# Kernel optimization log

Hardware: AMD Instinct MI355X
Metric: run time of the kernel (lower is better)

## Reference

```python
import jax, jax.numpy as jnp
import numpy as np

B, H, W, C = 1, 72, 72, 768
NH, HD = 12, 64
FF = 3072
EPS = 1e-6
THETA = 10000.0
S = H * W


def _rope_tables():
    freqs = 1.0 / THETA ** (np.arange(0, HD, 4, dtype=np.float32) / HD)  # [16]
    t = np.arange(H, dtype=np.float32)
    fx = np.outer(t, freqs)  # [72,16]
    fy = np.outer(t, freqs)
    fx = np.tile(fx[:, None, :], (1, W, 1))  # [72,72,16]
    fy = np.tile(fy[None, :, :], (H, 1, 1))
    fxy = np.concatenate([fx, fy], axis=-1).reshape(S, -1)  # [5184,32]
    fxy = np.repeat(fxy, 2, axis=-1)  # [5184,64]
    return jnp.asarray(np.cos(fxy)), jnp.asarray(np.sin(fxy))


def _rotate_pairwise(x):
    x1 = x[..., ::2]
    x2 = x[..., 1::2]
    return jnp.stack([-x2, x1], axis=-1).reshape(x.shape)


def _layernorm(x, g, b):
    m = jnp.mean(x, axis=-1, keepdims=True)
    v = jnp.mean(jnp.square(x - m), axis=-1, keepdims=True)
    return (x - m) * jax.lax.rsqrt(v + EPS) * g + b


def setup_inputs() -> dict:
    key = jax.random.key(0)
    ks = jax.random.split(key, 12)
    s_c = 1.0 / np.sqrt(C)
    s_ff = 1.0 / np.sqrt(FF)
    d = {
        "hidden_states": jax.random.normal(ks[0], (B, H, W, C), jnp.float32),
        "wq": jax.random.normal(ks[1], (C, C), jnp.float32) * s_c,
        "bq": jnp.zeros((C,), jnp.float32),
        "wk": jax.random.normal(ks[2], (C, C), jnp.float32) * s_c,
        "bk": jnp.zeros((C,), jnp.float32),
        "wv": jax.random.normal(ks[3], (C, C), jnp.float32) * s_c,
        "bv": jnp.zeros((C,), jnp.float32),
        "wo": jax.random.normal(ks[4], (C, C), jnp.float32) * s_c,
        "bo": jnp.zeros((C,), jnp.float32),
        "g1": jnp.ones((C,), jnp.float32),
        "b1": jnp.zeros((C,), jnp.float32),
        "g2": jnp.ones((C,), jnp.float32),
        "b2": jnp.zeros((C,), jnp.float32),
        "w_fc1": jax.random.normal(ks[5], (C, FF), jnp.float32) * s_c,
        "b_fc1": jnp.zeros((FF,), jnp.float32),
        "w_fc2": jax.random.normal(ks[6], (FF, C), jnp.float32) * s_ff,
        "b_fc2": jnp.zeros((C,), jnp.float32),
        "ls1": jnp.full((C,), 1e-5, jnp.float32),
        "ls2": jnp.full((C,), 1e-5, jnp.float32),
    }
    return d


def reference(hidden_states, wq, bq, wk, bk, wv, bv, wo, bo, g1, b1, g2, b2,
              w_fc1, b_fc1, w_fc2, b_fc2, ls1, ls2):
    cos, sin = _rope_tables()  # [S, HD]
    cos = cos[None, None]  # [1,1,S,HD]
    sin = sin[None, None]

    residual = hidden_states
    x = hidden_states.reshape(B, S, C)
    x = _layernorm(x, g1, b1)

    # attention
    q = (x @ wq + bq).reshape(B, S, NH, HD).transpose(0, 2, 1, 3)
    k = (x @ wk + bk).reshape(B, S, NH, HD).transpose(0, 2, 1, 3)
    v = (x @ wv + bv).reshape(B, S, NH, HD).transpose(0, 2, 1, 3)
    q = q * cos + _rotate_pairwise(q) * sin
    k = k * cos + _rotate_pairwise(k) * sin
    scale = HD ** -0.5
    attn = jax.nn.softmax(jnp.einsum('bhqd,bhkd->bhqk', q, k) * scale, axis=-1)
    o = jnp.einsum('bhqk,bhkd->bhqd', attn, v)
    o = o.transpose(0, 2, 1, 3).reshape(B, S, C)
    o = o @ wo + bo
    o = o * ls1

    hs = residual + o.reshape(B, H, W, C)
    residual = hs
    x = _layernorm(hs.reshape(B, S, C), g2, b2)
    x = jax.nn.gelu(x @ w_fc1 + b_fc1, approximate=False)
    x = x @ w_fc2 + b_fc2
    x = x * ls2
    return residual + x.reshape(B, H, W, C)
```

## Files before the change

kernel.cpp:

```cpp
#include <hip/hip_runtime.h>

#define S_  5184
#define C_  768
#define NH_ 12
#define HD_ 64
#define FF_ 3072
#define WW_ 72

typedef __attribute__((ext_vector_type(8))) short bf16x8;
typedef __attribute__((ext_vector_type(4))) float f32x4;

__device__ __forceinline__ float bf2f(unsigned short u){
    unsigned int i = ((unsigned int)u) << 16; float f; __builtin_memcpy(&f,&i,4); return f;
}
__device__ __forceinline__ unsigned short f2bf(float f){
    unsigned int i; __builtin_memcpy(&i,&f,4);
    unsigned int r = (i + 0x7fffu + ((i>>16)&1u)) >> 16;
    return (unsigned short)r;
}
__device__ __forceinline__ float ldf(float v){ return v; }
__device__ __forceinline__ float ldf(unsigned short v){ return bf2f(v); }

__device__ __forceinline__ void gload16(const void* g, const void* l) {
    __builtin_amdgcn_global_load_lds((const __attribute__((address_space(1))) void*)g,
                                     (__attribute__((address_space(3))) void*)l, 16, 0, 0);
}
__device__ __forceinline__ unsigned int cvtpk(float lo, float hi){
    unsigned int r;
    asm volatile("v_cvt_pk_bf16_f32 %0, %1, %2" : "=v"(r) : "v"(lo), "v"(hi));
    return r;
}

template<typename TIN>
__global__ __launch_bounds__(256) void ln_k(const TIN* __restrict__ x,
                                            const float* __restrict__ g,
                                            const float* __restrict__ b,
                                            unsigned short* __restrict__ out)
{
    int row = blockIdx.x, tid = threadIdx.x;
    const TIN* xr = x + (size_t)row * C_;
    float v0 = ldf(xr[tid]), v1 = ldf(xr[tid+256]), v2 = ldf(xr[tid+512]);
    float s = v0+v1+v2, q = v0*v0+v1*v1+v2*v2;
    #pragma unroll
    for (int off=32; off; off>>=1){ s += __shfl_xor(s,off); q += __shfl_xor(q,off); }
    __shared__ float ss[4], qq[4], mshare[2];
    int lane = tid & 63, wv = tid >> 6;
    if (!lane){ ss[wv] = s; qq[wv] = q; }
    __syncthreads();
    if (!tid){
        float S2 = ss[0]+ss[1]+ss[2]+ss[3];
        float Q2 = qq[0]+qq[1]+qq[2]+qq[3];
        float mean = S2 * (1.f/C_);
        float var  = Q2 * (1.f/C_) - mean*mean;
        mshare[0] = mean; mshare[1] = rsqrtf(var + 1e-6f);
    }
    __syncthreads();
    float mean = mshare[0], inv = mshare[1];
    unsigned short* orow = out + (size_t)row * C_;
    orow[tid]     = f2bf((v0-mean)*inv*g[tid]     + b[tid]);
    orow[tid+256] = f2bf((v1-mean)*inv*g[tid+256] + b[tid+256]);
    orow[tid+512] = f2bf((v2-mean)*inv*g[tid+512] + b[tid+512]);
}

__global__ __launch_bounds__(256) void rope_tables_k(float* __restrict__ cosT,
                                                     float* __restrict__ sinT)
{
    int idx = blockIdx.x * 256 + threadIdx.x;
    if (idx >= S_*32) return;
    int s = idx >> 5, i = idx & 31;
    int hh = s / WW_, ww = s % WW_;
    int m = i & 15;
    float coord = (i < 16) ? (float)hh : (float)ww;
    float freq = powf(10000.0f, -(float)m / 16.0f);
    float a = coord * freq;
    float c = cosf(a), sn = sinf(a);
    cosT[s*64 + 2*i]   = c;  cosT[s*64 + 2*i+1] = c;
    sinT[s*64 + 2*i]   = sn; sinT[s*64 + 2*i+1] = sn;
}

__global__ __launch_bounds__(256) void rope_apply_k(unsigned short* __restrict__ q,
                                                    unsigned short* __restrict__ k,
                                                    const float* __restrict__ cosT,
                                                    const float* __restrict__ sinT)
{
    int idx = blockIdx.x * 256 + threadIdx.x;
    if (idx >= S_*NH_*32) return;
    int s = idx / (NH_*32);
    int p = idx % (NH_*32);
    int h = p >> 5, i = p & 31;
    size_t base = (size_t)s*C_ + h*HD_ + 2*i;
    float c = cosT[s*64 + 2*i], sn = sinT[s*64 + 2*i];
    float x0 = bf2f(q[base]), x1 = bf2f(q[base+1]);
    q[base]   = f2bf((x0*c - x1*sn) * 0.125f);
    q[base+1] = f2bf((x1*c + x0*sn) * 0.125f);
    x0 = bf2f(k[base]); x1 = bf2f(k[base+1]);
    k[base]   = f2bf(x0*c - x1*sn);
    k[base+1] = f2bf(x1*c + x0*sn);
}

__global__ __launch_bounds__(256) void transpose_w(const float* __restrict__ W,
                                                   unsigned short* __restrict__ WT,
                                                   int K, int N)
{
    __shared__ float t[32][33];
    int tx = threadIdx.x, ty = threadIdx.y;
    int n0 = blockIdx.x * 32, k0 = blockIdx.y * 32;
    #pragma unroll
    for (int i = 0; i < 4; i++)
        t[ty + i*8][tx] = W[(size_t)(k0 + ty + i*8)*N + n0 + tx];
    __syncthreads();
    #pragma unroll
    for (int i = 0; i < 4; i++)
        WT[(size_t)(n0 + ty + i*8)*K + k0 + tx] = f2bf(t[tx][ty + i*8]);
}

template<int EPI, int NWC>
__global__ __launch_bounds__(256) void gemm_mfma(const unsigned short* __restrict__ A,
                                                 const unsigned short* __restrict__ BT,
                                                 const float* __restrict__ bias,
                                                 const float* __restrict__ biasB,
                                                 const float* __restrict__ biasC,
                                                 const float* __restrict__ scale,
                                                 const float* __restrict__ addend,
                                                 void* __restrict__ outp,
                                                 void* __restrict__ outp2,
                                                 int M, int N, int K)
{
    const int BN = 64*NWC;
    const int MI = (NWC == 2) ? 4 : 2;
    __shared__ __align__(16) unsigned short As[2][8192];
    __shared__ __align__(16) unsigned short Bs[2][4096*NWC];
    int tid = threadIdx.x;
    int w = tid >> 6, lane = tid & 63, lq = lane & 15, lk = lane >> 4;
    int wr = (NWC == 2) ? (w >> 1) : w;
    int wc = (NWC == 2) ? (w & 1) : 0;
    int bm = blockIdx.y * 128, bn = blockIdx.x * BN;

    f32x4 acc[MI][4];
    #pragma unroll
    for (int i = 0; i < MI; i++)
        #pragma unroll
        for (int j = 0; j < 4; j++) acc[i][j] = 0;

    auto STAGE = [&](int buf, int kt) {
        #pragma unroll
        for (int u = 0; u < 4; u++) {
            int t = w*4 + u;
            int c = t*64 + lane;
            int kg = c >> 7, row = c & 127;
            int ra = bm + row; if (ra >= M) ra = M - 1;
            gload16(A + (size_t)ra*K + kt*64 + kg*8, As[buf] + t*512);
        }
        #pragma unroll
        for (int u = 0; u < 2*NWC; u++) {
            int t = w*2*NWC + u;
            int c = t*64 + lane;
            int kg = (NWC == 2) ? (c >> 7) : (c >> 6);
            int row = (NWC == 2) ? (c & 127) : (c & 63);
            gload16(BT + (size_t)(bn + row)*K + kt*64 + kg*8, Bs[buf] + t*512);
        }
    };

    int nk = K / 64;
    STAGE(0, 0);
    int cur = 0;
    for (int kt = 0; kt < nk; kt++) {
        __syncthreads();
        if (kt + 1 < nk) STAGE(cur ^ 1, kt + 1);
        #pragma unroll
        for (int kk = 0; kk < 2; kk++) {
            bf16x8 af[MI], bfr[4];
            #pragma unroll
            for (int mi = 0; mi < MI; mi++)
                af[mi] = *(const bf16x8*)(As[cur] + (kk*4 + lk)*1024 + (wr*MI*16 + mi*16 + lq)*8);
            #pragma unroll
            for (int ni = 0; ni < 4; ni++)
                bfr[ni] = *(const bf16x8*)(Bs[cur] + (kk*4 + lk)*BN*8 + (wc*64 + ni*16 + lq)*8);
            #pragma unroll
            for (int mi = 0; mi < MI; mi++)
                #pragma unroll
                for (int ni = 0; ni < 4; ni++)
                    acc[mi][ni] = __builtin_amdgcn_mfma_f32_16x16x32_bf16(af[mi], bfr[ni], acc[mi][ni], 0, 0, 0);
        }
        cur ^= 1;
    }

    #pragma unroll
    for (int mi = 0; mi < MI; mi++) {
        #pragma unroll
        for (int ni = 0; ni < 4; ni++) {
            int n = bn + wc*64 + ni*16 + lq;
            int m0 = bm + wr*MI*16 + mi*16 + lk*4;
            if (EPI == 4) {
                if (n < 1536) {
                    const float* bb = (n < 768) ? bias : biasB;
                    int nn = (n < 768) ? n : (n - 768);
                    size_t base = (n < 768) ? 0 : ((size_t)S_ * 768);
                    #pragma unroll
                    for (int r = 0; r < 4; r++) {
                        int m = m0 + r;
                        if (m < M)
                            ((unsigned short*)outp)[base + (size_t)m*768 + nn] = f2bf(acc[mi][ni][r] + bb[nn]);
                    }
                } else {
                    if (m0 < M) {
                        float bv = biasC[n - 1536];
                        ushort4 pv;
                        pv.x = f2bf(acc[mi][ni][0] + bv);
                        pv.y = f2bf(acc[mi][ni][1] + bv);
                        pv.z = f2bf(acc[mi][ni][2] + bv);
                        pv.w = f2bf(acc[mi][ni][3] + bv);
                        *(ushort4*)((unsigned short*)outp2 + (size_t)(n - 1536)*S_ + m0) = pv;
                    }
                }
            } else {
                #pragma unroll
                for (int r = 0; r < 4; r++) {
                    int m = m0 + r;
                    if (m < M) {
                        float v = acc[mi][ni][r] + bias[n];
                        if (EPI == 1) {
                            v = 0.5f * v * (1.f + erff(v * 0.70710678f));
                            ((unsigned short*)outp)[(size_t)m*N + n] = f2bf(v);
                        } else {
                            size_t o = (size_t)m*N + n;
                            ((float*)outp)[o] = v*scale[n] + addend[o];
                        }
                    }
                }
            }
        }
    }
}

__global__ __launch_bounds__(256) void attn_mfma2(const unsigned short* __restrict__ Q,
                                                  const unsigned short* __restrict__ Kb,
                                                  const unsigned short* __restrict__ Vt,
                                                  unsigned short* __restrict__ O)
{
    __shared__ __align__(16) unsigned short Ks[2][4096];
    __shared__ __align__(16) unsigned short Vs[2][4096];
    int tid = threadIdx.x;
    int w = tid >> 6, lane = tid & 63, lq = lane & 15, lk = lane >> 4;
    int h = blockIdx.y;
    int q0 = blockIdx.x * 128 + w * 32;

    bf16x8 qf[2][2];
    #pragma unroll
    for (int qi = 0; qi < 2; qi++) {
        int qr = q0 + qi*16 + lq; if (qr >= S_) qr = S_ - 1;
        #pragma unroll
        for (int ks = 0; ks < 2; ks++)
            qf[qi][ks] = *(const bf16x8*)(Q + (size_t)qr*C_ + h*64 + ks*32 + lk*8);
    }

    f32x4 oacc[2][4];
    #pragma unroll
    for (int qi = 0; qi < 2; qi++)
        #pragma unroll
        for (int df = 0; df < 4; df++) oacc[qi][df] = 0;
    float m_[2] = {-INFINITY, -INFINITY};
    float l_[2] = {0.f, 0.f};

    auto STAGE = [&](int buf, int t) {
        int kv0 = t * 64;
        #pragma unroll
        for (int u = 0; u < 4; u++) {
            int tt = w*4 + u;
            if (tt < 8)
                gload16(Kb + (size_t)(kv0 + lane)*C_ + h*64 + tt*8, Ks[buf] + tt*512);
            else
                gload16(Vt + (size_t)(h*64 + lane)*S_ + kv0 + (tt-8)*8, Vs[buf] + (tt-8)*512);
        }
    };

    const int NT = S_/64;
    STAGE(0, 0);
    int cur = 0;
    for (int t = 0; t < NT; t++) {
        __syncthreads();
        if (t + 1 < NT) STAGE(cur ^ 1, t + 1);

        f32x4 s[2][4];
        #pragma unroll
        for (int qi = 0; qi < 2; qi++)
            #pragma unroll
            for (int nf = 0; nf < 4; nf++) s[qi][nf] = 0;
        #pragma unroll
        for (int ks = 0; ks < 2; ks++) {
            #pragma unroll
            for (int nf = 0; nf < 4; nf++) {
                bf16x8 kf = *(const bf16x8*)(Ks[cur] + (ks*4 + lk)*512 + (nf*16 + lq)*8);
                #pragma unroll
                for (int qi = 0; qi < 2; qi++)
                    s[qi][nf] = __builtin_amdgcn_mfma_f32_16x16x32_bf16(kf, qf[qi][ks], s[qi][nf], 0, 0, 0);
            }
        }

        unsigned int pk[2][8];
        #pragma unroll
        for (int qi = 0; qi < 2; qi++) {
            float tm = -INFINITY;
            #pragma unroll
            for (int nf = 0; nf < 4; nf++)
                #pragma unroll
                for (int r = 0; r < 4; r++) tm = fmaxf(tm, s[qi][nf][r]);
            tm = fmaxf(tm, __shfl_xor(tm, 16));
            tm = fmaxf(tm, __shfl_xor(tm, 32));
            float mn = fmaxf(m_[qi], tm);
            float corr = __expf(m_[qi] - mn);
            m_[qi] = mn;
            float ps = 0.f;
            #pragma unroll
            for (int nf = 0; nf < 4; nf++)
                #pragma unroll
                for (int r = 0; r < 4; r++) {
                    float p = __expf(s[qi][nf][r] - mn);
                    s[qi][nf][r] = p; ps += p;
                }
            ps += __shfl_xor(ps, 16);
            ps += __shfl_xor(ps, 32);
            l_[qi] = l_[qi]*corr + ps;
            #pragma unroll
            for (int df = 0; df < 4; df++)
                #pragma unroll
                for (int r = 0; r < 4; r++) oacc[qi][df][r] *= corr;
            #pragma unroll
            for (int nf = 0; nf < 4; nf++) {
                pk[qi][nf*2+0] = cvtpk(s[qi][nf][0], s[qi][nf][1]);
                pk[qi][nf*2+1] = cvtpk(s[qi][nf][2], s[qi][nf][3]);
            }
        }

        #pragma unroll
        for (int ks = 0; ks < 2; ks++) {
            #pragma unroll
            for (int df = 0; df < 4; df++) {
                int d = df*16 + lq;
                union { bf16x8 v; unsigned long long dd[2]; } va;
                va.dd[0] = *(const unsigned long long*)(Vs[cur] + (4*ks + (lk>>1))*512 + d*8 + (lk&1)*4);
                va.dd[1] = *(const unsigned long long*)(Vs[cur] + (4*ks + 2 + (lk>>1))*512 + d*8 + (lk&1)*4);
                #pragma unroll
                for (int qi = 0; qi < 2; qi++) {
                    union { bf16x8 v; unsigned int u[4]; } pb;
                    pb.u[0] = pk[qi][4*ks+0]; pb.u[1] = pk[qi][4*ks+1];
                    pb.u[2] = pk[qi][4*ks+2]; pb.u[3] = pk[qi][4*ks+3];
                    oacc[qi][df] = __builtin_amdgcn_mfma_f32_16x16x32_bf16(va.v, pb.v, oacc[qi][df], 0, 0, 0);
                }
            }
        }
        cur ^= 1;
    }

    #pragma unroll
    for (int qi = 0; qi < 2; qi++) {
        int q = q0 + qi*16 + lq;
        if (q < S_) {
            float rl = 1.f / l_[qi];
            #pragma unroll
            for (int df = 0; df < 4; df++) {
                ushort4 pv;
                pv.x = f2bf(oacc[qi][df][0] * rl);
                pv.y = f2bf(oacc[qi][df][1] * rl);
                pv.z = f2bf(oacc[qi][df][2] * rl);
                pv.w = f2bf(oacc[qi][df][3] * rl);
                *(ushort4*)(O + (size_t)q*C_ + h*64 + df*16 + lk*4) = pv;
            }
        }
    }
}

extern "C" void kernel_launch(void* const* d_in, const int* in_sizes, int n_in,
                              void* d_out, int out_size, void* d_ws, size_t ws_size,
                              hipStream_t stream)
{
    const float* hidden = (const float*)d_in[0];
    const float* wq  = (const float*)d_in[1];
    const float* bq  = (const float*)d_in[2];
    const float* wk  = (const float*)d_in[3];
    const float* bk  = (const float*)d_in[4];
    const float* wv  = (const float*)d_in[5];
    const float* bv  = (const float*)d_in[6];
    const float* wo  = (const float*)d_in[7];
    const float* bo  = (const float*)d_in[8];
    const float* g1  = (const float*)d_in[9];
    const float* b1  = (const float*)d_in[10];
    const float* g2  = (const float*)d_in[11];
    const float* b2  = (const float*)d_in[12];
    const float* wf1 = (const float*)d_in[13];
    const float* bf1 = (const float*)d_in[14];
    const float* wf2 = (const float*)d_in[15];
    const float* bf2_ = (const float*)d_in[16];
    const float* ls1 = (const float*)d_in[17];
    const float* ls2 = (const float*)d_in[18];

    char* ws = (char*)d_ws;
    size_t off = 0;
    auto alloc = [&](size_t bytes) { char* p = ws + off; off += (bytes + 255) & ~(size_t)255; return p; };

    float* res1          = (float*)alloc((size_t)S_*C_*4);
    float* cosT          = (float*)alloc((size_t)S_*64*4);
    float* sinT          = (float*)alloc((size_t)S_*64*4);
    unsigned short* lnb  = (unsigned short*)alloc((size_t)S_*C_*2);
    unsigned short* qb   = (unsigned short*)alloc((size_t)S_*C_*2);
    unsigned short* kb   = (unsigned short*)alloc((size_t)S_*C_*2);
    unsigned short* vtb  = (unsigned short*)alloc((size_t)S_*C_*2);
    unsigned short* ob   = (unsigned short*)alloc((size_t)S_*C_*2);
    unsigned short* fc1b = qb;
    unsigned short* wqT  = (unsigned short*)alloc((size_t)C_*C_*2);
    unsigned short* wkT  = (unsigned short*)alloc((size_t)C_*C_*2);
    unsigned short* wvT  = (unsigned short*)alloc((size_t)C_*C_*2);
    unsigned short* woT  = (unsigned short*)alloc((size_t)C_*C_*2);
    unsigned short* wf1T = (unsigned short*)alloc((size_t)C_*FF_*2);
    unsigned short* wf2T = (unsigned short*)alloc((size_t)C_*FF_*2);
    float* outb = (float*)d_out;

    hipLaunchKernelGGL(transpose_w, dim3(C_/32, C_/32), dim3(32,8), 0, stream, wq,  wqT,  C_, C_);
    hipLaunchKernelGGL(transpose_w, dim3(C_/32, C_/32), dim3(32,8), 0, stream, wk,  wkT,  C_, C_);
    hipLaunchKernelGGL(transpose_w, dim3(C_/32, C_/32), dim3(32,8), 0, stream, wv,  wvT,  C_, C_);
    hipLaunchKernelGGL(transpose_w, dim3(C_/32, C_/32), dim3(32,8), 0, stream, wo,  woT,  C_, C_);
    hipLaunchKernelGGL(transpose_w, dim3(FF_/32, C_/32), dim3(32,8), 0, stream, wf1, wf1T, C_, FF_);
    hipLaunchKernelGGL(transpose_w, dim3(C_/32, FF_/32), dim3(32,8), 0, stream, wf2, wf2T, FF_, C_);
    hipLaunchKernelGGL(ln_k<float>, dim3(S_), dim3(256), 0, stream, hidden, g1, b1, lnb);
    hipLaunchKernelGGL(rope_tables_k, dim3((S_*32 + 255)/256), dim3(256), 0, stream, cosT, sinT);
    hipLaunchKernelGGL((gemm_mfma<4,2>), dim3(2304/128, 41), dim3(256), 0, stream,
                       lnb, wqT, bq, bk, bv, (const float*)nullptr, (const float*)nullptr,
                       (void*)qb, (void*)vtb, S_, 2304, C_);
    hipLaunchKernelGGL(rope_apply_k, dim3((S_*NH_*32 + 255)/256), dim3(256), 0, stream,
                       qb, kb, cosT, sinT);
    hipLaunchKernelGGL(attn_mfma2, dim3((S_ + 127)/128, NH_), dim3(256), 0, stream, qb, kb, vtb, ob);
    hipLaunchKernelGGL((gemm_mfma<2,1>), dim3(C_/64, 41), dim3(256), 0, stream,
                       ob, woT, bo, (const float*)nullptr, (const float*)nullptr, ls1, hidden,
                       (void*)res1, (void*)nullptr, S_, C_, C_);
    hipLaunchKernelGGL(ln_k<float>, dim3(S_), dim3(256), 0, stream, res1, g2, b2, lnb);
    hipLaunchKernelGGL((gemm_mfma<1,2>), dim3(FF_/128, 41), dim3(256), 0, stream,
                       lnb, wf1T, bf1, (const float*)nullptr, (const float*)nullptr,
                       (const float*)nullptr, (const float*)nullptr,
                       (void*)fc1b, (void*)nullptr, S_, FF_, C_);
    hipLaunchKernelGGL((gemm_mfma<2,1>), dim3(C_/64, 41), dim3(256), 0, stream,
                       fc1b, wf2T, bf2_, (const float*)nullptr, (const float*)nullptr, ls2, res1,
                       (void*)outb, (void*)nullptr, S_, C_, FF_);
    (void)in_sizes; (void)n_in; (void)out_size; (void)ws_size;
}
```

Baseline: 477.8 us.

## Shrink attention tiles, use exp2 softmax with lazy rescale, remap GEMM blocks per XCD

The attention kernel now gives each wave 16 query rows instead of 32 and launches 81x12 blocks instead of 41x12, which raises occupancy and spreads work across more CUs, though each staged K/V tile is reused by fewer queries. The softmax folds log2(e) into the Q scale so it can use exp2f, and it skips the running-max rescale of the output accumulators when no lane's max increases. GEMM block indices are remapped so that consecutive tiles land on the same XCD, aiming for better L2 reuse. The cost is twice the K/V global and LDS traffic per query, since K/V tiles are shared by half as many queries.

```diff
diff --git a/kernel.cpp b/kernel.cpp
--- a/kernel.cpp
+++ b/kernel.cpp
@@ -89,10 +89,11 @@
     int p = idx % (NH_*32);
     int h = p >> 5, i = p & 31;
     size_t base = (size_t)s*C_ + h*HD_ + 2*i;
+    const float QS = 0.18033688011112042f;
     float c = cosT[s*64 + 2*i], sn = sinT[s*64 + 2*i];
     float x0 = bf2f(q[base]), x1 = bf2f(q[base+1]);
-    q[base]   = f2bf((x0*c - x1*sn) * 0.125f);
-    q[base+1] = f2bf((x1*c + x0*sn) * 0.125f);
+    q[base]   = f2bf((x0*c - x1*sn) * QS);
+    q[base+1] = f2bf((x1*c + x0*sn) * QS);
     x0 = bf2f(k[base]); x1 = bf2f(k[base+1]);
     k[base]   = f2bf(x0*c - x1*sn);
     k[base+1] = f2bf(x1*c + x0*sn);
@@ -134,7 +135,14 @@
     int w = tid >> 6, lane = tid & 63, lq = lane & 15, lk = lane >> 4;
     int wr = (NWC == 2) ? (w >> 1) : w;
     int wc = (NWC == 2) ? (w & 1) : 0;
-    int bm = blockIdx.y * 128, bn = blockIdx.x * BN;
+
+    int gx = gridDim.x;
+    int nwg = gx * gridDim.y;
+    int bid = blockIdx.y * gx + blockIdx.x;
+    int xcd = bid & 7, idx = bid >> 3;
+    int qq = nwg >> 3, rr = nwg & 7;
+    int wg = (xcd < rr) ? (xcd*(qq+1) + idx) : (rr*(qq+1) + (xcd-rr)*qq + idx);
+    int bm = (wg / gx) * 128, bn = (wg % gx) * BN;
 
     f32x4 acc[MI][4];
     #pragma unroll
@@ -233,7 +241,7 @@
     }
 }
 
-__global__ __launch_bounds__(256) void attn_mfma2(const unsigned short* __restrict__ Q,
+__global__ __launch_bounds__(256) void attn_mfma3(const unsigned short* __restrict__ Q,
                                                   const unsigned short* __restrict__ Kb,
                                                   const unsigned short* __restrict__ Vt,
                                                   unsigned short* __restrict__ O)
@@ -243,24 +251,17 @@
     int tid = threadIdx.x;
     int w = tid >> 6, lane = tid & 63, lq = lane & 15, lk = lane >> 4;
     int h = blockIdx.y;
-    int q0 = blockIdx.x * 128 + w * 32;
-
-    bf16x8 qf[2][2];
-    #pragma unroll
-    for (int qi = 0; qi < 2; qi++) {
-        int qr = q0 + qi*16 + lq; if (qr >= S_) qr = S_ - 1;
-        #pragma unroll
-        for (int ks = 0; ks < 2; ks++)
-            qf[qi][ks] = *(const bf16x8*)(Q + (size_t)qr*C_ + h*64 + ks*32 + lk*8);
-    }
-
-    f32x4 oacc[2][4];
-    #pragma unroll
-    for (int qi = 0; qi < 2; qi++)
-        #pragma unroll
-        for (int df = 0; df < 4; df++) oacc[qi][df] = 0;
-    float m_[2] = {-INFINITY, -INFINITY};
-    float l_[2] = {0.f, 0.f};
+    int q0 = blockIdx.x * 64 + w * 16;
+
+    bf16x8 qf[2];
+    #pragma unroll
+    for (int ks = 0; ks < 2; ks++)
+        qf[ks] = *(const bf16x8*)(Q + (size_t)(q0 + lq)*C_ + h*64 + ks*32 + lk*8);
+
+    f32x4 oacc[4];
+    #pragma unroll
+    for (int df = 0; df < 4; df++) oacc[df] = 0;
+    float m_ = -INFINITY, l_ = 0.f;
 
     auto STAGE = [&](int buf, int t) {
         int kv0 = t * 64;
@@ -281,92 +282,81 @@
         __syncthreads();
         if (t + 1 < NT) STAGE(cur ^ 1, t + 1);
 
-        f32x4 s[2][4];
-        #pragma unroll
-        for (int qi = 0; qi < 2; qi++)
-            #pragma unroll
-            for (int nf = 0; nf < 4; nf++) s[qi][nf] = 0;
+        f32x4 s[4];
+        #pragma unroll
+        for (int nf = 0; nf < 4; nf++) s[nf] = 0;
         #pragma unroll
         for (int ks = 0; ks < 2; ks++) {
             #pragma unroll
             for (int nf = 0; nf < 4; nf++) {
                 bf16x8 kf = *(const bf16x8*)(Ks[cur] + (ks*4 + lk)*512 + (nf*16 + lq)*8);
-                #pragma unroll
-                for (int qi = 0; qi < 2; qi++)
-                    s[qi][nf] = __builtin_amdgcn_mfma_f32_16x16x32_bf16(kf, qf[qi][ks], s[qi][nf], 0, 0, 0);
+                s[nf] = __builtin_amdgcn_mfma_f32_16x16x32_bf16(kf, qf[ks], s[nf], 0, 0, 0);
             }
         }
 
-        unsigned int pk[2][8];
-        #pragma unroll
-        for (int qi = 0; qi < 2; qi++) {
-            float tm = -INFINITY;
-            #pragma unroll
-            for (int nf = 0; nf < 4; nf++)
-                #pragma unroll
-                for (int r = 0; r < 4; r++) tm = fmaxf(tm, s[qi][nf][r]);
-            tm = fmaxf(tm, __shfl_xor(tm, 16));
-            tm = fmaxf(tm, __shfl_xor(tm, 32));
-            float mn = fmaxf(m_[qi], tm);
-            float corr = __expf(m_[qi] - mn);
-            m_[qi] = mn;
-            float ps = 0.f;
-            #pragma unroll
-            for (int nf = 0; nf < 4; nf++)
-                #pragma unroll
-                for (int r = 0; r < 4; r++) {
-                    float p = __expf(s[qi][nf][r] - mn);
-                    s[qi][nf][r] = p; ps += p;
-                }
-            ps += __shfl_xor(ps, 16);
-            ps += __shfl_xor(ps, 32);
-            l_[qi] = l_[qi]*corr + ps;
+        float tm = -INFINITY;
+        #pragma unroll
+        for (int nf = 0; nf < 4; nf++)
+            #pragma unroll
+            for (int r = 0; r < 4; r++) tm = fmaxf(tm, s[nf][r]);
+        tm = fmaxf(tm, __shfl_xor(tm, 16));
+        tm = fmaxf(tm, __shfl_xor(tm, 32));
+        if (__any(tm > m_)) {
+            float mn = fmaxf(m_, tm);
+            float corr = exp2f(m_ - mn);
+            m_ = mn;
+            l_ *= corr;
             #pragma unroll
             for (int df = 0; df < 4; df++)
                 #pragma unroll
-                for (int r = 0; r < 4; r++) oacc[qi][df][r] *= corr;
-            #pragma unroll
-            for (int nf = 0; nf < 4; nf++) {
-                pk[qi][nf*2+0] = cvtpk(s[qi][nf][0], s[qi][nf][1]);
-                pk[qi][nf*2+1] = cvtpk(s[qi][nf][2], s[qi][nf][3]);
+                for (int r = 0; r < 4; r++) oacc[df][r] *= corr;
+        }
+        float ps = 0.f;
+        #pragma unroll
+        for (int nf = 0; nf < 4; nf++)
+            #pragma unroll
+            for (int r = 0; r < 4; r++) {
+                float p = exp2f(s[nf][r] - m_);
+                s[nf][r] = p; ps += p;
             }
+        ps += __shfl_xor(ps, 16);
+        ps += __shfl_xor(ps, 32);
+        l_ += ps;
+
+        unsigned int pk[8];
+        #pragma unroll
+        for (int nf = 0; nf < 4; nf++) {
+            pk[nf*2+0] = cvtpk(s[nf][0], s[nf][1]);
+            pk[nf*2+1] = cvtpk(s[nf][2], s[nf][3]);
         }
 
         #pragma unroll
         for (int ks = 0; ks < 2; ks++) {
+            union { bf16x8 v; unsigned int u[4]; } pb;
+            pb.u[0] = pk[4*ks+0]; pb.u[1] = pk[4*ks+1];
+            pb.u[2] = pk[4*ks+2]; pb.u[3] = pk[4*ks+3];
             #pragma unroll
             for (int df = 0; df < 4; df++) {
                 int d = df*16 + lq;
                 union { bf16x8 v; unsigned long long dd[2]; } va;
                 va.dd[0] = *(const unsigned long long*)(Vs[cur] + (4*ks + (lk>>1))*512 + d*8 + (lk&1)*4);
                 va.dd[1] = *(const unsigned long long*)(Vs[cur] + (4*ks + 2 + (lk>>1))*512 + d*8 + (lk&1)*4);
-                #pragma unroll
-                for (int qi = 0; qi < 2; qi++) {
-                    union { bf16x8 v; unsigned int u[4]; } pb;
-                    pb.u[0] = pk[qi][4*ks+0]; pb.u[1] = pk[qi][4*ks+1];
-                    pb.u[2] = pk[qi][4*ks+2]; pb.u[3] = pk[qi][4*ks+3];
-                    oacc[qi][df] = __builtin_amdgcn_mfma_f32_16x16x32_bf16(va.v, pb.v, oacc[qi][df], 0, 0, 0);
-                }
+                oacc[df] = __builtin_amdgcn_mfma_f32_16x16x32_bf16(va.v, pb.v, oacc[df], 0, 0, 0);
             }
         }
         cur ^= 1;
     }
 
-    #pragma unroll
-    for (int qi = 0; qi < 2; qi++) {
-        int q = q0 + qi*16 + lq;
-        if (q < S_) {
-            float rl = 1.f / l_[qi];
-            #pragma unroll
-            for (int df = 0; df < 4; df++) {
-                ushort4 pv;
-                pv.x = f2bf(oacc[qi][df][0] * rl);
-                pv.y = f2bf(oacc[qi][df][1] * rl);
-                pv.z = f2bf(oacc[qi][df][2] * rl);
-                pv.w = f2bf(oacc[qi][df][3] * rl);
-                *(ushort4*)(O + (size_t)q*C_ + h*64 + df*16 + lk*4) = pv;
-            }
-        }
+    float rl = 1.f / l_;
+    int q = q0 + lq;
+    #pragma unroll
+    for (int df = 0; df < 4; df++) {
+        ushort4 pv;
+        pv.x = f2bf(oacc[df][0] * rl);
+        pv.y = f2bf(oacc[df][1] * rl);
+        pv.z = f2bf(oacc[df][2] * rl);
+        pv.w = f2bf(oacc[df][3] * rl);
+        *(ushort4*)(O + (size_t)q*C_ + h*64 + df*16 + lk*4) = pv;
     }
 }
 
@@ -428,7 +418,7 @@
                        (void*)qb, (void*)vtb, S_, 2304, C_);
     hipLaunchKernelGGL(rope_apply_k, dim3((S_*NH_*32 + 255)/256), dim3(256), 0, stream,
                        qb, kb, cosT, sinT);
-    hipLaunchKernelGGL(attn_mfma2, dim3((S_ + 127)/128, NH_), dim3(256), 0, stream, qb, kb, vtb, ob);
+    hipLaunchKernelGGL(attn_mfma3, dim3(S_/64, NH_), dim3(256), 0, stream, qb, kb, vtb, ob);
     hipLaunchKernelGGL((gemm_mfma<2,1>), dim3(C_/64, 41), dim3(256), 0, stream,
                        ob, woT, bo, (const float*)nullptr, (const float*)nullptr, ls1, hidden,
                        (void*)res1, (void*)nullptr, S_, C_, C_);
```

Measured after the change: 507.0 us. 6.1% more time.
